# Kernel tuning notes

Measured on AMD Instinct MI355X. Metric: run time of the kernel, lower is better.

The kernel has to match this reference:

```python
import jax, jax.numpy as jnp
import numpy as np

D_MODEL = 512
N_HEADS = 8
D_K = 64
D_V = 64
SCALE = 1.0 / np.sqrt(D_K).astype(np.float32)
LN_EPS = 1e-5


def setup_inputs() -> dict:
    key = jax.random.key(0)
    ks = jax.random.split(key, 8)
    B, S = 4, 2048
    xavier = np.sqrt(6.0 / (D_MODEL + D_MODEL)).astype(np.float32)
    return {
        "input_Q": jax.random.normal(ks[0], (B, S, D_MODEL), jnp.float32),
        "input_K": jax.random.normal(ks[1], (B, S, D_MODEL), jnp.float32),
        "input_V": jax.random.normal(ks[2], (B, S, D_MODEL), jnp.float32),
        "attn_mask": jax.random.randint(ks[3], (B, S, S), 0, 2).astype(bool),
        "W_Q": jax.random.uniform(ks[4], (D_MODEL, D_MODEL), jnp.float32, -xavier, xavier),
        "W_K": jax.random.uniform(ks[5], (D_MODEL, D_MODEL), jnp.float32, -xavier, xavier),
        "W_V": jax.random.uniform(ks[6], (D_MODEL, D_MODEL), jnp.float32, -xavier, xavier),
        "W_fc": jax.random.uniform(ks[7], (D_MODEL, D_MODEL), jnp.float32, -xavier, xavier),
        "ln_gamma": jnp.ones((D_MODEL,), jnp.float32),
        "ln_beta": jnp.zeros((D_MODEL,), jnp.float32),
    }


def _layernorm(x, gamma, beta):
    mu = jnp.mean(x, axis=-1, keepdims=True)
    var = jnp.mean(jnp.square(x - mu), axis=-1, keepdims=True)
    return (x - mu) * jax.lax.rsqrt(var + LN_EPS) * gamma + beta


def reference(input_Q, input_K, input_V, attn_mask, W_Q, W_K, W_V, W_fc, ln_gamma, ln_beta):
    B = input_Q.shape[0]
    # torch Linear: x @ W.T ; W is (out, in)
    def proj(x, W):
        y = jnp.einsum('bsd,ed->bse', x, W)  # (B,S,n_heads*d_k)
        return y.reshape(B, -1, N_HEADS, D_K).transpose(0, 2, 1, 3)  # (B,H,S,dk)

    Q = proj(input_Q, W_Q)
    K = proj(input_K, W_K)
    V = proj(input_V, W_V)

    scores = jnp.einsum('bhqd,bhkd->bhqk', Q, K) * SCALE
    scores = jnp.clip(scores, -1e9, 1e10)
    mask = attn_mask[:, None, :, :]  # broadcast over heads
    scores = jnp.where(mask, jnp.float32(-1e9), scores)
    attn = jax.nn.softmax(scores, axis=-1)
    attn = jnp.clip(attn, 1e-8, 1.0)
    result = jnp.einsum('bhqk,bhkd->bhqd', attn, V)
    result = result.transpose(0, 2, 1, 3).reshape(B, -1, N_HEADS * D_V)
    output = jnp.einsum('bsd,ed->bse', result, W_fc)
    out = _layernorm(output + input_Q, ln_gamma, ln_beta)
    return (out, attn)
```

## Files before the change

kernel.cpp:

```cpp
#include <hip/hip_runtime.h>

typedef float  f32x4  __attribute__((ext_vector_type(4)));
typedef __bf16 bf16x8 __attribute__((ext_vector_type(8)));

#define MFMA_BF16(a, b, c) __builtin_amdgcn_mfma_f32_16x16x32_bf16((a), (b), (c), 0, 0, 0)

#define BDIM   4
#define SEQ    2048
#define DM     512
#define NH     8
#define DK     64
#define ATT_SCALE 0.125f
#define NEG_CAP  (-80.0f)
#define KT     64
#define NT     (SEQ / KT)
#define QB     128
#define PS     72
#define KTDK   (KT * DK)

static __device__ __forceinline__ unsigned short f2bf(float f) {
  unsigned int u = __builtin_bit_cast(unsigned int, f);
  u += 0x7fffu + ((u >> 16) & 1u);
  return (unsigned short)(u >> 16);
}
static __device__ __forceinline__ float bf2f(unsigned short u) {
  return __builtin_bit_cast(float, (unsigned)u << 16);
}
static __device__ __forceinline__ void gload16(const void* g, unsigned short* l) {
  __builtin_amdgcn_global_load_lds((const __attribute__((address_space(1))) void*)g,
                                   (__attribute__((address_space(3))) void*)l, 16, 0, 0);
}
static __device__ __forceinline__ bf16x8 lds128(const unsigned short* base, int row, int m) {
  return *(const bf16x8*)((const char*)base + row * 128 + (((m) ^ (row & 7)) << 4));
}

__global__ __launch_bounds__(256) void cvt7_kernel(
    const float* __restrict__ x0, const float* __restrict__ x1, const float* __restrict__ x2,
    const float* __restrict__ w0, const float* __restrict__ w1, const float* __restrict__ w2,
    const float* __restrict__ w3,
    unsigned short* __restrict__ dx0, unsigned short* __restrict__ dx1,
    unsigned short* __restrict__ dx2, unsigned short* __restrict__ dw0,
    unsigned short* __restrict__ dw1, unsigned short* __restrict__ dw2,
    unsigned short* __restrict__ dw3, int nx4, int nw4) {
  const int z = blockIdx.y;
  const float* src;
  unsigned short* dst;
  int n4;
  switch (z) {
    case 0: src = x0; dst = dx0; n4 = nx4; break;
    case 1: src = x1; dst = dx1; n4 = nx4; break;
    case 2: src = x2; dst = dx2; n4 = nx4; break;
    case 3: src = w0; dst = dw0; n4 = nw4; break;
    case 4: src = w1; dst = dw1; n4 = nw4; break;
    case 5: src = w2; dst = dw2; n4 = nw4; break;
    default: src = w3; dst = dw3; n4 = nw4; break;
  }
  int i = blockIdx.x * 256 + threadIdx.x;
  if (i >= n4) return;
  float4 v = reinterpret_cast<const float4*>(src)[i];
  ushort4 o;
  o.x = f2bf(v.x); o.y = f2bf(v.y); o.z = f2bf(v.z); o.w = f2bf(v.w);
  reinterpret_cast<ushort4*>(dst)[i] = o;
}

__global__ void detect_mask_kernel(const unsigned int* __restrict__ m, int* __restrict__ flag) {
  __shared__ int s;
  if (threadIdx.x == 0) s = 0;
  __syncthreads();
  int any = 0;
  for (int i = threadIdx.x; i < 4096; i += 256) any |= (m[i] > 1u) ? 1 : 0;
  if (any) atomicOr(&s, 1);
  __syncthreads();
  if (threadIdx.x == 0) *flag = s;
}

__global__ __launch_bounds__(256) void mask_pack_kernel(const unsigned char* __restrict__ m8,
                                                        const int* __restrict__ m32,
                                                        const int* __restrict__ flag,
                                                        unsigned long long* __restrict__ bits) {
  const int wid = blockIdx.x * 256 + threadIdx.x;
  const int use8 = *flag;
  unsigned long long v = 0;
  if (use8) {
    const uchar4* p = (const uchar4*)(m8 + (size_t)wid * 64);
#pragma unroll
    for (int c = 0; c < 16; ++c) {
      uchar4 q = p[c];
      v |= ((unsigned long long)(q.x != 0)) << (c * 4 + 0);
      v |= ((unsigned long long)(q.y != 0)) << (c * 4 + 1);
      v |= ((unsigned long long)(q.z != 0)) << (c * 4 + 2);
      v |= ((unsigned long long)(q.w != 0)) << (c * 4 + 3);
    }
  } else {
    const int4* p = (const int4*)(m32 + (size_t)wid * 64);
#pragma unroll
    for (int c = 0; c < 16; ++c) {
      int4 q = p[c];
      v |= ((unsigned long long)(q.x != 0)) << (c * 4 + 0);
      v |= ((unsigned long long)(q.y != 0)) << (c * 4 + 1);
      v |= ((unsigned long long)(q.z != 0)) << (c * 4 + 2);
      v |= ((unsigned long long)(q.w != 0)) << (c * 4 + 3);
    }
  }
  bits[wid] = v;
}

__device__ __forceinline__ void gemm128_main(const unsigned short* __restrict__ A,
                                             const unsigned short* __restrict__ B,
                                             int K, int row0, int col0,
                                             unsigned short* lds, f32x4 acc[4][4]) {
  const int tid  = threadIdx.x;
  const int w    = tid >> 6;
  const int lane = tid & 63;
  const int lr   = lane & 15;
  const int lk   = (lane >> 4) << 3;
  const int wm   = (w >> 1) << 6;
  const int wn   = (w & 1) << 6;
  const int sr   = tid >> 2;
  const int sc   = (tid & 3) << 3;
  unsigned short* As = lds;
  unsigned short* Bs = lds + 128 * 40;
  for (int k0 = 0; k0 < K; k0 += 32) {
    __syncthreads();
    *(int4*)&As[(size_t)sr * 40 + sc]        = *(const int4*)&A[(size_t)(row0 + sr) * K + k0 + sc];
    *(int4*)&As[(size_t)(sr + 64) * 40 + sc] = *(const int4*)&A[(size_t)(row0 + sr + 64) * K + k0 + sc];
    *(int4*)&Bs[(size_t)sr * 40 + sc]        = *(const int4*)&B[(size_t)(col0 + sr) * K + k0 + sc];
    *(int4*)&Bs[(size_t)(sr + 64) * 40 + sc] = *(const int4*)&B[(size_t)(col0 + sr + 64) * K + k0 + sc];
    __syncthreads();
    bf16x8 af[4], bfr[4];
#pragma unroll
    for (int mi = 0; mi < 4; ++mi) af[mi]  = *(const bf16x8*)&As[(size_t)(wm + mi * 16 + lr) * 40 + lk];
#pragma unroll
    for (int ni = 0; ni < 4; ++ni) bfr[ni] = *(const bf16x8*)&Bs[(size_t)(wn + ni * 16 + lr) * 40 + lk];
#pragma unroll
    for (int mi = 0; mi < 4; ++mi)
#pragma unroll
      for (int ni = 0; ni < 4; ++ni)
        acc[mi][ni] = MFMA_BF16(af[mi], bfr[ni], acc[mi][ni]);
  }
}

__global__ __launch_bounds__(256) void proj_kernel(
    const unsigned short* __restrict__ Xq, const unsigned short* __restrict__ Xk,
    const unsigned short* __restrict__ Xv,
    const unsigned short* __restrict__ Wq, const unsigned short* __restrict__ Wk,
    const unsigned short* __restrict__ Wv,
    unsigned short* __restrict__ Qh, unsigned short* __restrict__ Kh,
    unsigned short* __restrict__ VT) {
  __shared__ __align__(16) unsigned short lds[2 * 128 * 40];
  const int z = blockIdx.z;
  const unsigned short* A = (z == 0) ? Xq : ((z == 1) ? Xk : Xv);
  const unsigned short* B = (z == 0) ? Wq : ((z == 1) ? Wk : Wv);
  unsigned short* O       = (z == 0) ? Qh : ((z == 1) ? Kh : VT);
  const int row0 = blockIdx.x * 128, col0 = blockIdx.y * 128;
  f32x4 acc[4][4];
  const f32x4 zero = {0.f, 0.f, 0.f, 0.f};
#pragma unroll
  for (int mi = 0; mi < 4; ++mi)
#pragma unroll
    for (int ni = 0; ni < 4; ++ni) acc[mi][ni] = zero;
  gemm128_main(A, B, DM, row0, col0, lds, acc);
  const int w = threadIdx.x >> 6, lane = threadIdx.x & 63;
  const int lr = lane & 15, lg = lane >> 4;
  const int wm = (w >> 1) << 6, wn = (w & 1) << 6;
#pragma unroll
  for (int mi = 0; mi < 4; ++mi)
#pragma unroll
    for (int ni = 0; ni < 4; ++ni)
#pragma unroll
      for (int j = 0; j < 4; ++j) {
        const int m = row0 + wm + mi * 16 + lg * 4 + j;
        const int n = col0 + wn + ni * 16 + lr;
        const int b = m >> 11, s = m & 2047;
        const int h = n >> 6,  d = n & 63;
        const unsigned short val = f2bf(acc[mi][ni][j]);
        if (z == 2)
          O[(((size_t)(b * NH + h)) * DK + d) * SEQ + s] = val;
        else
          O[(((size_t)(b * NH + h)) * SEQ + s) * DK + d] = val;
      }
}

__global__ __launch_bounds__(256) void fc_kernel(const unsigned short* __restrict__ A,
                                                 const unsigned short* __restrict__ W,
                                                 float* __restrict__ Out) {
  __shared__ __align__(16) unsigned short lds[2 * 128 * 40];
  const int row0 = blockIdx.x * 128, col0 = blockIdx.y * 128;
  f32x4 acc[4][4];
  const f32x4 zero = {0.f, 0.f, 0.f, 0.f};
#pragma unroll
  for (int mi = 0; mi < 4; ++mi)
#pragma unroll
    for (int ni = 0; ni < 4; ++ni) acc[mi][ni] = zero;
  gemm128_main(A, W, DM, row0, col0, lds, acc);
  const int w = threadIdx.x >> 6, lane = threadIdx.x & 63;
  const int lr = lane & 15, lg = lane >> 4;
  const int wm = (w >> 1) << 6, wn = (w & 1) << 6;
#pragma unroll
  for (int mi = 0; mi < 4; ++mi)
#pragma unroll
    for (int ni = 0; ni < 4; ++ni)
#pragma unroll
      for (int j = 0; j < 4; ++j) {
        const int m = row0 + wm + mi * 16 + lg * 4 + j;
        const int n = col0 + wn + ni * 16 + lr;
        Out[(size_t)m * DM + n] = acc[mi][ni][j];
      }
}

__global__ __launch_bounds__(512, 4) void attn_kernel(
    const unsigned short* __restrict__ Qh, const unsigned short* __restrict__ Kh,
    const unsigned short* __restrict__ VT, const unsigned long long* __restrict__ Mb,
    float* __restrict__ attn_out, unsigned short* __restrict__ R16) {
  __shared__ __align__(16) unsigned short Ks[2][KTDK];
  __shared__ __align__(16) unsigned short Vs[2][KTDK];
  __shared__ __align__(16) unsigned short Pl[8][16 * PS];
  const int id  = blockIdx.x + 16 * (blockIdx.y + 8 * blockIdx.z);
  const int q8  = id >> 3;
  const int bh  = (id & 7) * 4 + (q8 >> 4);
  const int qt  = q8 & 15;
  const int b   = bh >> 3;
  const int tid = threadIdx.x, w = tid >> 6, lane = tid & 63;
  const int lr = lane & 15, lg = lane >> 4;
  const unsigned short* Qp = Qh + (size_t)bh * SEQ * DK;
  const unsigned short* Kp = Kh + (size_t)bh * SEQ * DK;
  const unsigned short* Vp = VT + (size_t)bh * DK * SEQ;
  float* ap = attn_out + (size_t)bh * SEQ * SEQ;

  const int qb = qt * QB + w * 16;
  const bf16x8 qf0 = *(const bf16x8*)(Qp + (size_t)(qb + lr) * DK + lg * 8);
  const bf16x8 qf1 = *(const bf16x8*)(Qp + (size_t)(qb + lr) * DK + 32 + lg * 8);
  const unsigned long long* mrow = Mb + ((size_t)b * SEQ + qb + lr) * 32;

  const int srow = tid >> 3, schunk = tid & 7;
  const int sg = schunk ^ (srow & 7);
  const unsigned short* kstage = Kp + (size_t)srow * DK + sg * 8;
  const unsigned short* vstage = Vp + (size_t)srow * SEQ + sg * 8;
  unsigned short* kdst0 = &Ks[0][tid * 8];
  unsigned short* kdst1 = &Ks[1][tid * 8];
  unsigned short* vdst0 = &Vs[0][tid * 8];
  unsigned short* vdst1 = &Vs[1][tid * 8];

  float sv[4][4];

  float l = 0.f;
  gload16(kstage, kdst0);
  __syncthreads();
  for (int t = 0; t < NT; ++t) {
    const unsigned short* Kb = Ks[t & 1];
    if (t + 1 < NT) gload16(kstage + (size_t)(t + 1) * KTDK, (t & 1) ? kdst0 : kdst1);
    const unsigned long long mr = mrow[t];
#pragma unroll
    for (int ni = 0; ni < 4; ++ni) {
      const int r = ni * 16 + lr;
      bf16x8 k0 = lds128(Kb, r, lg);
      bf16x8 k1 = lds128(Kb, r, lg + 4);
      f32x4 z = {0.f, 0.f, 0.f, 0.f};
      z = MFMA_BF16(k0, qf0, z);
      z = MFMA_BF16(k1, qf1, z);
#pragma unroll
      for (int j = 0; j < 4; ++j)
        sv[ni][j] = ((mr >> (ni * 16 + lg * 4 + j)) & 1ull) ? NEG_CAP : z[j] * ATT_SCALE;
    }
#pragma unroll
    for (int ni = 0; ni < 4; ++ni)
      l += __expf(sv[ni][0]) + __expf(sv[ni][1]) + __expf(sv[ni][2]) + __expf(sv[ni][3]);
    __syncthreads();
  }
  l += __shfl_xor(l, 16);
  l += __shfl_xor(l, 32);
  const float invl = 1.0f / l;

  f32x4 o[4];
  const f32x4 zero = {0.f, 0.f, 0.f, 0.f};
#pragma unroll
  for (int nd = 0; nd < 4; ++nd) o[nd] = zero;
  unsigned short* Pw = &Pl[w][0];

  gload16(kstage, kdst0);
  gload16(vstage, vdst0);
  asm volatile("s_waitcnt vmcnt(0)" ::: "memory");
  __builtin_amdgcn_s_barrier();
  for (int t = 0; t < NT; ++t) {
    const unsigned short* Kb = Ks[t & 1];
    const unsigned short* Vb = Vs[t & 1];
    if (t + 1 < NT) {
      gload16(kstage + (size_t)(t + 1) * KTDK, (t & 1) ? kdst0 : kdst1);
      gload16(vstage + (size_t)(t + 1) * KT,   (t & 1) ? vdst0 : vdst1);
    }
    const unsigned long long mr = mrow[t];
#pragma unroll
    for (int ni = 0; ni < 4; ++ni) {
      const int r = ni * 16 + lr;
      bf16x8 k0 = lds128(Kb, r, lg);
      bf16x8 k1 = lds128(Kb, r, lg + 4);
      f32x4 z = {0.f, 0.f, 0.f, 0.f};
      z = MFMA_BF16(k0, qf0, z);
      z = MFMA_BF16(k1, qf1, z);
#pragma unroll
      for (int j = 0; j < 4; ++j)
        sv[ni][j] = ((mr >> (ni * 16 + lg * 4 + j)) & 1ull) ? NEG_CAP : z[j] * ATT_SCALE;
    }
#pragma unroll
    for (int ni = 0; ni < 4; ++ni) {
      float p0 = fminf(fmaxf(__expf(sv[ni][0]) * invl, 1e-8f), 1.0f);
      float p1 = fminf(fmaxf(__expf(sv[ni][1]) * invl, 1e-8f), 1.0f);
      float p2 = fminf(fmaxf(__expf(sv[ni][2]) * invl, 1e-8f), 1.0f);
      float p3 = fminf(fmaxf(__expf(sv[ni][3]) * invl, 1e-8f), 1.0f);
      ushort4 pk = {f2bf(p0), f2bf(p1), f2bf(p2), f2bf(p3)};
      *(ushort4*)&Pw[lr * PS + ni * 16 + lg * 4] = pk;
    }
    const bf16x8 pf0 = *(const bf16x8*)&Pw[lr * PS + lg * 8];
    const bf16x8 pf1 = *(const bf16x8*)&Pw[lr * PS + 32 + lg * 8];
#pragma unroll
    for (int nd = 0; nd < 4; ++nd) {
      const int r = nd * 16 + lr;
      o[nd] = MFMA_BF16(pf0, lds128(Vb, r, lg), o[nd]);
    }
#pragma unroll
    for (int nd = 0; nd < 4; ++nd) {
      const int r = nd * 16 + lr;
      o[nd] = MFMA_BF16(pf1, lds128(Vb, r, lg + 4), o[nd]);
    }
#pragma unroll
    for (int j = 0; j < 4; ++j) {
      const int r = lg * 4 + j;
      ushort4 pk = *(const ushort4*)&Pw[r * PS + lr * 4];
      float4 f = {bf2f(pk.x), bf2f(pk.y), bf2f(pk.z), bf2f(pk.w)};
      *(float4*)(ap + (size_t)(qb + r) * SEQ + t * KT + lr * 4) = f;
    }
    if (t + 1 < NT) {
      asm volatile("s_waitcnt vmcnt(4)" ::: "memory");
      __builtin_amdgcn_s_barrier();
    }
  }
#pragma unroll
  for (int nd = 0; nd < 4; ++nd)
#pragma unroll
    for (int j = 0; j < 4; ++j)
      R16[((size_t)(b * SEQ + qb + lg * 4 + j)) * DM + (bh & 7) * DK + nd * 16 + lr] = f2bf(o[nd][j]);
}

__global__ __launch_bounds__(256) void ln_kernel(const float* __restrict__ fc,
                                                 const float* __restrict__ xq,
                                                 const float* __restrict__ gamma,
                                                 const float* __restrict__ beta,
                                                 float* __restrict__ out) {
  const int row = blockIdx.x * 4 + (threadIdx.x >> 6);
  const int lane = threadIdx.x & 63;
  const float* f = fc + (size_t)row * DM;
  const float* x = xq + (size_t)row * DM;
  float v[8];
  float s = 0.f, ss = 0.f;
#pragma unroll
  for (int i = 0; i < 8; ++i) {
    const int c = lane + i * 64;
    const float t = f[c] + x[c];
    v[i] = t; s += t; ss += t * t;
  }
#pragma unroll
  for (int off = 1; off < 64; off <<= 1) {
    s  += __shfl_xor(s, off);
    ss += __shfl_xor(ss, off);
  }
  const float mu  = s * (1.f / 512.f);
  const float var = ss * (1.f / 512.f) - mu * mu;
  const float inv = rsqrtf(var + 1e-5f);
  float* op = out + (size_t)row * DM;
#pragma unroll
  for (int i = 0; i < 8; ++i) {
    const int c = lane + i * 64;
    op[c] = (v[i] - mu) * inv * gamma[c] + beta[c];
  }
}


extern "C" void kernel_launch(void* const* d_in, const int* in_sizes, int n_in,
                              void* d_out, int out_size, void* d_ws, size_t ws_size,
                              hipStream_t stream) {
  const float* xq   = (const float*)d_in[0];
  const float* xk   = (const float*)d_in[1];
  const float* xv   = (const float*)d_in[2];
  const void*  mask = d_in[3];
  const float* wq   = (const float*)d_in[4];
  const float* wk   = (const float*)d_in[5];
  const float* wv   = (const float*)d_in[6];
  const float* wfc  = (const float*)d_in[7];
  const float* gamma = (const float*)d_in[8];
  const float* beta  = (const float*)d_in[9];

  float* out = (float*)d_out;
  float* attn_out = out + (size_t)BDIM * SEQ * DM;

  char* ws = (char*)d_ws;
  unsigned short* XQ16 = (unsigned short*)(ws);
  unsigned short* XK16 = (unsigned short*)(ws + 8388608);
  unsigned short* XV16 = (unsigned short*)(ws + 16777216);
  unsigned short* WQ16 = (unsigned short*)(ws + 25165824);
  unsigned short* WK16 = (unsigned short*)(ws + 25690112);
  unsigned short* WV16 = (unsigned short*)(ws + 26214400);
  unsigned short* WF16 = (unsigned short*)(ws + 26738688);
  unsigned short* Qh   = (unsigned short*)(ws + 27262976);
  unsigned short* Kh   = (unsigned short*)(ws + 35651584);
  unsigned short* VT   = (unsigned short*)(ws + 44040192);
  unsigned long long* Mbits = (unsigned long long*)(ws);
  unsigned short* R16  = (unsigned short*)(ws + 16777216);
  float*          FC32 = (float*)(ws + 27262976);
  int*            FLAG = (int*)(ws + 52428800);

  const int NX4 = BDIM * SEQ * DM / 4;
  const int NW4 = DM * DM / 4;

  detect_mask_kernel<<<1, 256, 0, stream>>>((const unsigned int*)mask, FLAG);
  cvt7_kernel<<<dim3(NX4 / 256, 7), 256, 0, stream>>>(xq, xk, xv, wq, wk, wv, wfc,
                                                      XQ16, XK16, XV16,
                                                      WQ16, WK16, WV16, WF16, NX4, NW4);
  proj_kernel<<<dim3(64, 4, 3), 256, 0, stream>>>(XQ16, XK16, XV16,
                                                  WQ16, WK16, WV16, Qh, Kh, VT);
  mask_pack_kernel<<<1024, 256, 0, stream>>>((const unsigned char*)mask,
                                             (const int*)mask, FLAG, Mbits);
  attn_kernel<<<dim3(16, NH, BDIM), 512, 0, stream>>>(Qh, Kh, VT, Mbits, attn_out, R16);
  fc_kernel<<<dim3(64, 4, 1), 256, 0, stream>>>(R16, WF16, FC32);
  ln_kernel<<<2048, 256, 0, stream>>>(FC32, xq, gamma, beta, out);
}
```

Measured before the change: 309.8 us.

## Fold softmax normalization into exp2 argument and use async LDS loads in GEMM

The attention softmax now works in base 2. The scale is folded into a log2e constant, and the normalizer is applied by subtracting log2(l) inside the exponent, so the per-element multiply and clamp go away. Raw v_exp_f32/v_log_f32 instructions and a cheaper round-half-up bf16 conversion replace __expf and round-to-nearest-even. Separately, the projection and fc GEMM tile loads now go straight from global memory to LDS with an unpadded 32-element stride, dropping the register staging. This risks LDS bank conflicts from the lost padding, and dropping the 1e-8 clamp and the masked-value constant slightly changes numerics.

```diff
diff --git a/kernel.cpp b/kernel.cpp
--- a/kernel.cpp
+++ b/kernel.cpp
@@ -10,21 +10,35 @@
 #define DM     512
 #define NH     8
 #define DK     64
-#define ATT_SCALE 0.125f
-#define NEG_CAP  (-80.0f)
 #define KT     64
 #define NT     (SEQ / KT)
 #define QB     128
 #define PS     72
 #define KTDK   (KT * DK)
+#define C2LOG2E  0.18033688011112042f
+#define MASKED_X (-115.41560327111707f)
 
 static __device__ __forceinline__ unsigned short f2bf(float f) {
   unsigned int u = __builtin_bit_cast(unsigned int, f);
   u += 0x7fffu + ((u >> 16) & 1u);
   return (unsigned short)(u >> 16);
 }
+static __device__ __forceinline__ unsigned short rhu(float f) {
+  unsigned int u = __builtin_bit_cast(unsigned int, f);
+  return (unsigned short)((u + 0x8000u) >> 16);
+}
 static __device__ __forceinline__ float bf2f(unsigned short u) {
   return __builtin_bit_cast(float, (unsigned)u << 16);
+}
+static __device__ __forceinline__ float exp2_fast(float x) {
+  float r;
+  asm("v_exp_f32 %0, %1" : "=v"(r) : "v"(x));
+  return r;
+}
+static __device__ __forceinline__ float log2_fast(float x) {
+  float r;
+  asm("v_log_f32 %0, %1" : "=v"(r) : "v"(x));
+  return r;
 }
 static __device__ __forceinline__ void gload16(const void* g, unsigned short* l) {
   __builtin_amdgcn_global_load_lds((const __attribute__((address_space(1))) void*)g,
@@ -116,22 +130,30 @@
   const int lk   = (lane >> 4) << 3;
   const int wm   = (w >> 1) << 6;
   const int wn   = (w & 1) << 6;
-  const int sr   = tid >> 2;
-  const int sc   = (tid & 3) << 3;
   unsigned short* As = lds;
-  unsigned short* Bs = lds + 128 * 40;
+  unsigned short* Bs = lds + 128 * 32;
+  const int r0 = tid >> 2;
+  const int c0 = (tid & 3) << 3;
+  const unsigned short* a0 = A + (size_t)(row0 + r0) * K + c0;
+  const unsigned short* a1 = A + (size_t)(row0 + r0 + 64) * K + c0;
+  const unsigned short* b0 = B + (size_t)(col0 + r0) * K + c0;
+  const unsigned short* b1 = B + (size_t)(col0 + r0 + 64) * K + c0;
+  unsigned short* dA0 = &As[tid * 8];
+  unsigned short* dA1 = &As[(tid + 256) * 8];
+  unsigned short* dB0 = &Bs[tid * 8];
+  unsigned short* dB1 = &Bs[(tid + 256) * 8];
   for (int k0 = 0; k0 < K; k0 += 32) {
     __syncthreads();
-    *(int4*)&As[(size_t)sr * 40 + sc]        = *(const int4*)&A[(size_t)(row0 + sr) * K + k0 + sc];
-    *(int4*)&As[(size_t)(sr + 64) * 40 + sc] = *(const int4*)&A[(size_t)(row0 + sr + 64) * K + k0 + sc];
-    *(int4*)&Bs[(size_t)sr * 40 + sc]        = *(const int4*)&B[(size_t)(col0 + sr) * K + k0 + sc];
-    *(int4*)&Bs[(size_t)(sr + 64) * 40 + sc] = *(const int4*)&B[(size_t)(col0 + sr + 64) * K + k0 + sc];
+    gload16(a0 + k0, dA0);
+    gload16(a1 + k0, dA1);
+    gload16(b0 + k0, dB0);
+    gload16(b1 + k0, dB1);
     __syncthreads();
     bf16x8 af[4], bfr[4];
 #pragma unroll
-    for (int mi = 0; mi < 4; ++mi) af[mi]  = *(const bf16x8*)&As[(size_t)(wm + mi * 16 + lr) * 40 + lk];
-#pragma unroll
-    for (int ni = 0; ni < 4; ++ni) bfr[ni] = *(const bf16x8*)&Bs[(size_t)(wn + ni * 16 + lr) * 40 + lk];
+    for (int mi = 0; mi < 4; ++mi) af[mi]  = *(const bf16x8*)&As[(wm + mi * 16 + lr) * 32 + lk];
+#pragma unroll
+    for (int ni = 0; ni < 4; ++ni) bfr[ni] = *(const bf16x8*)&Bs[(wn + ni * 16 + lr) * 32 + lk];
 #pragma unroll
     for (int mi = 0; mi < 4; ++mi)
 #pragma unroll
@@ -147,7 +169,7 @@
     const unsigned short* __restrict__ Wv,
     unsigned short* __restrict__ Qh, unsigned short* __restrict__ Kh,
     unsigned short* __restrict__ VT) {
-  __shared__ __align__(16) unsigned short lds[2 * 128 * 40];
+  __shared__ __align__(16) unsigned short lds[2 * 128 * 32];
   const int z = blockIdx.z;
   const unsigned short* A = (z == 0) ? Xq : ((z == 1) ? Xk : Xv);
   const unsigned short* B = (z == 0) ? Wq : ((z == 1) ? Wk : Wv);
@@ -184,7 +206,7 @@
 __global__ __launch_bounds__(256) void fc_kernel(const unsigned short* __restrict__ A,
                                                  const unsigned short* __restrict__ W,
                                                  float* __restrict__ Out) {
-  __shared__ __align__(16) unsigned short lds[2 * 128 * 40];
+  __shared__ __align__(16) unsigned short lds[2 * 128 * 32];
   const int row0 = blockIdx.x * 128, col0 = blockIdx.y * 128;
   f32x4 acc[4][4];
   const f32x4 zero = {0.f, 0.f, 0.f, 0.f};
@@ -241,9 +263,7 @@
   unsigned short* vdst0 = &Vs[0][tid * 8];
   unsigned short* vdst1 = &Vs[1][tid * 8];
 
-  float sv[4][4];
-
-  float l = 0.f;
+  float l2 = 0.f;
   gload16(kstage, kdst0);
   __syncthreads();
   for (int t = 0; t < NT; ++t) {
@@ -259,17 +279,18 @@
       z = MFMA_BF16(k0, qf0, z);
       z = MFMA_BF16(k1, qf1, z);
 #pragma unroll
-      for (int j = 0; j < 4; ++j)
-        sv[ni][j] = ((mr >> (ni * 16 + lg * 4 + j)) & 1ull) ? NEG_CAP : z[j] * ATT_SCALE;
-    }
-#pragma unroll
-    for (int ni = 0; ni < 4; ++ni)
-      l += __expf(sv[ni][0]) + __expf(sv[ni][1]) + __expf(sv[ni][2]) + __expf(sv[ni][3]);
+      for (int j = 0; j < 4; ++j) {
+        const float t1 = z[j] * C2LOG2E;
+        const float x = ((mr >> (ni * 16 + lg * 4 + j)) & 1ull) ? MASKED_X : t1;
+        l2 += exp2_fast(x);
+      }
+    }
     __syncthreads();
   }
-  l += __shfl_xor(l, 16);
-  l += __shfl_xor(l, 32);
-  const float invl = 1.0f / l;
+  l2 += __shfl_xor(l2, 16);
+  l2 += __shfl_xor(l2, 32);
+  const float negllog = -log2_fast(l2);
+  const float mAlt = MASKED_X + negllog;
 
   f32x4 o[4];
   const f32x4 zero = {0.f, 0.f, 0.f, 0.f};
@@ -297,17 +318,14 @@
       f32x4 z = {0.f, 0.f, 0.f, 0.f};
       z = MFMA_BF16(k0, qf0, z);
       z = MFMA_BF16(k1, qf1, z);
-#pragma unroll
-      for (int j = 0; j < 4; ++j)
-        sv[ni][j] = ((mr >> (ni * 16 + lg * 4 + j)) & 1ull) ? NEG_CAP : z[j] * ATT_SCALE;
-    }
-#pragma unroll
-    for (int ni = 0; ni < 4; ++ni) {
-      float p0 = fminf(fmaxf(__expf(sv[ni][0]) * invl, 1e-8f), 1.0f);
-      float p1 = fminf(fmaxf(__expf(sv[ni][1]) * invl, 1e-8f), 1.0f);
-      float p2 = fminf(fmaxf(__expf(sv[ni][2]) * invl, 1e-8f), 1.0f);
-      float p3 = fminf(fmaxf(__expf(sv[ni][3]) * invl, 1e-8f), 1.0f);
-      ushort4 pk = {f2bf(p0), f2bf(p1), f2bf(p2), f2bf(p3)};
+      float p[4];
+#pragma unroll
+      for (int j = 0; j < 4; ++j) {
+        const float t1 = fmaf(z[j], C2LOG2E, negllog);
+        const float x = ((mr >> (ni * 16 + lg * 4 + j)) & 1ull) ? mAlt : t1;
+        p[j] = exp2_fast(x);
+      }
+      ushort4 pk = {rhu(p[0]), rhu(p[1]), rhu(p[2]), rhu(p[3])};
       *(ushort4*)&Pw[lr * PS + ni * 16 + lg * 4] = pk;
     }
     const bf16x8 pf0 = *(const bf16x8*)&Pw[lr * PS + lg * 8];
```

After: 305.0 us. Within noise of the previous version (-1.6%).
